# Kernel tuning notes

Measured on AMD Instinct MI355X. Metric: run time of the kernel, lower is better.

Reference implementation:

```python
import jax, jax.numpy as jnp
import numpy as np

B, N, D = 8, 2048, 256
K = 16384  # codebook_size


def setup_inputs() -> dict:
    key = jax.random.key(0)
    k1, k2, k3, k4 = jax.random.split(key, 4)
    z = jax.random.normal(k1, (B, N, D), dtype=jnp.float32)
    emb_weight = jax.random.normal(k2, (K, D), dtype=jnp.float32) * 0.02
    proj_w = jax.random.normal(k3, (D, D), dtype=jnp.float32) * (1.0 / np.sqrt(D))
    proj_b = jax.random.normal(k4, (D,), dtype=jnp.float32) * 0.01
    return {"z": z, "emb_weight": emb_weight, "proj_w": proj_w, "proj_b": proj_b}


def reference(z, emb_weight, proj_w, proj_b):
    # emb = embedding_proj(embedding.weight)  (torch Linear: x @ W^T + b)
    emb = emb_weight @ proj_w.T + proj_b  # (K, D)
    b, n, d = z.shape
    zf = z.reshape(b * n, d)  # (BN, D)
    # squared euclidean distances: ||z||^2 + ||e||^2 - 2 z e^T
    dist = (
        jnp.sum(zf * zf, axis=1, keepdims=True)
        + jnp.sum(emb * emb, axis=1)
        - 2.0 * jnp.einsum("bd,kd->bk", zf, emb)
    )  # (BN, K)
    q_indices = jnp.argmin(dist, axis=1)  # (BN,) int
    quantized = emb[q_indices].reshape(z.shape)  # (B, N, D)
    # straight-through estimator
    quantized = z + jax.lax.stop_gradient(quantized - z)
    q_indices = q_indices.reshape(b, n)
    # (unregularized_z, emb, regularized_z, bottleneck_rep)
    return z, emb, quantized, q_indices
```

## Files before the change

kernel.cpp:

```cpp
#include <hip/hip_runtime.h>
#include <hip/hip_bf16.h>

#define D      256
#define KCB    16384
#define BNROWS 16384
#define NT     4
#define MARGIN 0.15f
#define BIAS   8.0f
#define ZMAX   5.0f
#define EMAX   0.2f

typedef __attribute__((ext_vector_type(4))) int   int4v;
typedef __attribute__((ext_vector_type(4))) float f32x4;
typedef unsigned long long u64;

__device__ __forceinline__ void gload_lds16(const void* g, void* l) {
    __builtin_amdgcn_global_load_lds(
        (const __attribute__((address_space(1))) void*)g,
        (__attribute__((address_space(3))) void*)l, 16, 0, 0);
}

__device__ __forceinline__ unsigned fmap(float f) {
    unsigned u = __float_as_uint(f);
    return (u & 0x80000000u) ? ~u : (u | 0x80000000u);
}

__device__ __forceinline__ signed char q8(float x, float s) {
    return (signed char)__float2int_rn(fminf(fmaxf(x * s, -127.f), 127.f));
}

__global__ __launch_bounds__(256) void zquant_kernel(
    const float* __restrict__ z, signed char* __restrict__ z8)
{
    const int i = blockIdx.x * 256 + threadIdx.x;
    float4 v = ((const float4*)z)[i];
    const float s = 127.0f / ZMAX;
    char4 c;
    c.x = q8(v.x, s); c.y = q8(v.y, s); c.z = q8(v.z, s); c.w = q8(v.w, s);
    ((char4*)z8)[i] = c;
}

__global__ __launch_bounds__(256) void proj_kernel(
    const float* __restrict__ ew, const float* __restrict__ pw,
    const float* __restrict__ pb, float* __restrict__ emb)
{
    __shared__ float Et[64][65];
    __shared__ float Pt[64][65];
    const int tid = threadIdx.x;
    const int tc  = tid & 15, tr = tid >> 4;
    const int k0  = (blockIdx.x >> 2) * 64;
    const int d0  = (blockIdx.x & 3) * 64;

    float acc[4][4];
#pragma unroll
    for (int a = 0; a < 4; ++a)
#pragma unroll
        for (int b = 0; b < 4; ++b) acc[a][b] = 0.f;

    for (int j0 = 0; j0 < 256; j0 += 64) {
        __syncthreads();
#pragma unroll
        for (int i = 0; i < 4; ++i) {
            const int c = i * 256 + tid;
            const int r = c >> 4, c4 = (c & 15) * 4;
            float4 v = *(const float4*)(ew + (size_t)(k0 + r) * 256 + j0 + c4);
            Et[r][c4 + 0] = v.x; Et[r][c4 + 1] = v.y;
            Et[r][c4 + 2] = v.z; Et[r][c4 + 3] = v.w;
            float4 w = *(const float4*)(pw + (size_t)(d0 + r) * 256 + j0 + c4);
            Pt[r][c4 + 0] = w.x; Pt[r][c4 + 1] = w.y;
            Pt[r][c4 + 2] = w.z; Pt[r][c4 + 3] = w.w;
        }
        __syncthreads();
        for (int j = 0; j < 64; ++j) {
            float ev[4], pv[4];
#pragma unroll
            for (int a = 0; a < 4; ++a) ev[a] = Et[tr * 4 + a][j];
#pragma unroll
            for (int b = 0; b < 4; ++b) pv[b] = Pt[tc * 4 + b][j];
#pragma unroll
            for (int a = 0; a < 4; ++a)
#pragma unroll
                for (int b = 0; b < 4; ++b)
                    acc[a][b] = fmaf(ev[a], pv[b], acc[a][b]);
        }
    }

    const float4 bias = *(const float4*)(pb + d0 + tc * 4);
#pragma unroll
    for (int a = 0; a < 4; ++a) {
        float4 o;
        o.x = acc[a][0] + bias.x; o.y = acc[a][1] + bias.y;
        o.z = acc[a][2] + bias.z; o.w = acc[a][3] + bias.w;
        *(float4*)(emb + (size_t)(k0 + tr * 4 + a) * 256 + d0 + tc * 4) = o;
    }
}

__global__ __launch_bounds__(256) void snorm_equant_kernel(
    const float* __restrict__ emb, float* __restrict__ s,
    float* __restrict__ s8b, signed char* __restrict__ e8)
{
    const int tid = threadIdx.x;
    const int row = blockIdx.x * 64 + (tid >> 2);
    const int qd  = tid & 3;
    const size_t base = (size_t)row * 256;
    const float se = 127.0f / EMAX;
    float sq = 0.f;
#pragma unroll
    for (int j = 0; j < 16; ++j) {
        const int off = qd * 4 + j * 16;
        float4 v = *(const float4*)(emb + base + off);
        char4 c;
        c.x = q8(v.x, se); c.y = q8(v.y, se);
        c.z = q8(v.z, se); c.w = q8(v.w, se);
        *(char4*)(e8 + base + off) = c;
        sq = fmaf(v.x, v.x, fmaf(v.y, v.y, fmaf(v.z, v.z, fmaf(v.w, v.w, sq))));
    }
    sq += __shfl_xor(sq, 1);
    sq += __shfl_xor(sq, 2);
    if (qd == 0) {
        s[row]   = sq;
        s8b[row] = sq + BIAS;
    }
}

__global__ __launch_bounds__(512, 4) void argmin_hi_kernel(
    const signed char* __restrict__ z8, const signed char* __restrict__ e8,
    const float* __restrict__ s8b,
    unsigned* __restrict__ partial1, unsigned* __restrict__ partial2)
{
    __shared__ alignas(16) short A_lds[3 * 4096];
    __shared__ alignas(16) short B_lds[3 * 8192];

    const int tid  = threadIdx.x;
    const int lane = tid & 63;
    const int wid  = tid >> 6;
    const int wz   = wid >> 2;
    const int wc   = wid & 3;
    const int lcol = lane & 15;
    const int rhi  = lane >> 4;

    const int bm = blockIdx.x >> 6;
    const int bn = blockIdx.x & 63;
    const size_t r0 = (size_t)bm * 128;
    const size_t n0 = (size_t)bn * 256;

    const int slot  = (((lcol & 1) * 4 + rhi) ^ ((lcol >> 1) & 7)) << 3;
    const int aoff0 = wz * 2048 + (lcol >> 1) * 64 + slot;
    const int boff0 = wc * 2048 + (lcol >> 1) * 64 + slot;

    auto goff = [](int c) {
        const int l = c >> 3, u = (c & 7) ^ (l & 7);
        return (size_t)(2 * l + (u >> 2)) * 256 + (size_t)(u & 3) * 16;
    };
    const size_t gA  = goff(tid);
    const int    cB0 = wid * 128 + lane;
    const int    cB1 = cB0 + 64;
    const size_t gB0 = goff(cB0);
    const size_t gB1 = goff(cB1);

    short* const aDst  = A_lds + tid * 8;
    short* const bDst0 = B_lds + cB0 * 8;
    short* const bDst1 = B_lds + cB1 * 8;

    const char* const z8B = (const char*)z8 + r0 * 256;
    const char* const e8B = (const char*)e8 + n0 * 256;

    gload_lds16(z8B + gA, aDst);
    gload_lds16(e8B + gB0, bDst0);
    gload_lds16(e8B + gB1, bDst1);
    gload_lds16(z8B + 64 + gA, aDst + 4096);
    gload_lds16(e8B + 64 + gB0, bDst0 + 8192);
    gload_lds16(e8B + 64 + gB1, bDst1 + 8192);
    asm volatile("s_waitcnt vmcnt(3)" ::: "memory");
    __builtin_amdgcn_s_barrier();

    int4v acc[4][4];
    const int4v izero = {0, 0, 0, 0};
#pragma unroll
    for (int m = 0; m < 4; ++m)
#pragma unroll
        for (int n = 0; n < 4; ++n) acc[m][n] = izero;

#define TILE_BODY(JL)                                                         \
    {                                                                         \
        const int t  = i3 + (JL);                                             \
        const int tp = t + 2;                                                 \
        int4v bq[4];                                                          \
        _Pragma("unroll")                                                     \
        for (int n = 0; n < 4; ++n)            \
            bq[n] = *(const int4v*)(A_lds + (JL) * 4096 + aoff0 + n * 512);   \
        if (tp < NT) {                                                        \
            const char* Ab = z8B + ((size_t)tp << 6);                         \
            const char* Bb = e8B + ((size_t)tp << 6);                         \
            gload_lds16(Ab + gA, aDst + (((JL) + 2) % 3) * 4096);             \
            gload_lds16(Bb + gB0, bDst0 + (((JL) + 2) % 3) * 8192);           \
            gload_lds16(Bb + gB1, bDst1 + (((JL) + 2) % 3) * 8192);           \
        }                                                                     \
        __builtin_amdgcn_s_setprio(1);                                        \
        _Pragma("unroll")                                                     \
        for (int m = 0; m < 4; ++m) {       \
            const int4v am = *(const int4v*)(B_lds + (JL) * 8192 + boff0 + m * 512); \
            _Pragma("unroll")                                                 \
            for (int n = 0; n < 4; ++n)                                       \
                acc[m][n] = __builtin_amdgcn_mfma_i32_16x16x64_i8(            \
                    am, bq[n], acc[m][n], 0, 0, 0);                           \
        }                                                                     \
        __builtin_amdgcn_s_setprio(0);                                        \
        if (tp < NT)                                                          \
            asm volatile("s_waitcnt vmcnt(3)" ::: "memory");                  \
        else if (t + 1 < NT)                                                  \
            asm volatile("s_waitcnt vmcnt(0)" ::: "memory");                  \
        __builtin_amdgcn_s_barrier();                                         \
    }

    {
        const int i3 = 0;
        TILE_BODY(0)
        TILE_BODY(1)
        TILE_BODY(2)
    }
    {
        const int i3 = 3;
        TILE_BODY(0)
    }
#undef TILE_BODY

    const float FS2 = -2.0f * (ZMAX / 127.0f) * (EMAX / 127.0f);
    float4 s8[4];
#pragma unroll
    for (int mc = 0; mc < 4; ++mc)
        s8[mc] = *(const float4*)(s8b + n0 + wc * 64 + mc * 16 + rhi * 4);

    u64* cand = (u64*)A_lds;
#pragma unroll
    for (int nz = 0; nz < 4; ++nz) {
        unsigned v[16];
#pragma unroll
        for (int mc = 0; mc < 4; ++mc) {
            const unsigned cb = (unsigned)(wc * 64 + mc * 16 + rhi * 4);
            v[mc * 4 + 0] = (__float_as_uint(fmaf(FS2, (float)acc[mc][nz][0], s8[mc].x)) & 0xFFFFFF00u) | (cb + 0);
            v[mc * 4 + 1] = (__float_as_uint(fmaf(FS2, (float)acc[mc][nz][1], s8[mc].y)) & 0xFFFFFF00u) | (cb + 1);
            v[mc * 4 + 2] = (__float_as_uint(fmaf(FS2, (float)acc[mc][nz][2], s8[mc].z)) & 0xFFFFFF00u) | (cb + 2);
            v[mc * 4 + 3] = (__float_as_uint(fmaf(FS2, (float)acc[mc][nz][3], s8[mc].w)) & 0xFFFFFF00u) | (cb + 3);
        }
        unsigned p1 = min(v[0], v[1]), p2 = max(v[0], v[1]);
#pragma unroll
        for (int i = 1; i < 8; ++i) {
            const unsigned l = min(v[2 * i], v[2 * i + 1]);
            const unsigned h = max(v[2 * i], v[2 * i + 1]);
            const unsigned t = max(p1, l);
            p1 = min(p1, l);
            p2 = min(t, min(p2, h));
        }
#pragma unroll
        for (int mask = 16; mask <= 32; mask <<= 1) {
            const unsigned q1 = __shfl_xor(p1, mask);
            const unsigned q2 = __shfl_xor(p2, mask);
            const unsigned t  = max(p1, q1);
            p1 = min(p1, q1);
            p2 = min(t, min(p2, q2));
        }
        if (rhi == 0) {
            const int row = wz * 64 + nz * 16 + lcol;
            cand[row * 4 + wc] = (u64)p1 | ((u64)p2 << 32);
        }
    }
    __syncthreads();
    if (tid < 128) {
        const u64* c4 = cand + (size_t)tid * 4;
        u64 a = c4[0];
        unsigned p1 = (unsigned)a, p2 = (unsigned)(a >> 32);
#pragma unroll
        for (int w = 1; w < 4; ++w) {
            a = c4[w];
            const unsigned q1 = (unsigned)a, q2 = (unsigned)(a >> 32);
            const unsigned t  = max(p1, q1);
            p1 = min(p1, q1);
            p2 = min(t, min(p2, q2));
        }
        partial1[(size_t)bn * BNROWS + r0 + tid] = p1;
        partial2[(size_t)bn * BNROWS + r0 + tid] = p2;
    }
}

__global__ __launch_bounds__(256) void collect_rescore_kernel(
    const unsigned* __restrict__ partial1, const unsigned* __restrict__ partial2,
    const float* __restrict__ z, const float* __restrict__ emb,
    const float* __restrict__ s,
    float* __restrict__ outz, float* __restrict__ outq,
    float* __restrict__ outidx)
{
    __shared__ unsigned gsb;
    __shared__ int      nsel;
    __shared__ int      selk[128];
    __shared__ u64      wbest[4];
    __shared__ int      kfin;

    const int tid  = threadIdx.x;
    const int row  = blockIdx.x;
    const int lane = tid & 63;
    const int wid  = tid >> 6;

    unsigned v = 0xFFFFFFFFu;
    int vbn = 0;
    if (tid < 64)       { v = partial1[(size_t)tid * BNROWS + row];        vbn = tid; }
    else if (tid < 128) { v = partial2[(size_t)(tid - 64) * BNROWS + row]; vbn = tid - 64; }

    if (tid < 64) {
        unsigned g = v;
#pragma unroll
        for (int mm = 1; mm < 64; mm <<= 1) g = min(g, (unsigned)__shfl_xor(g, mm));
        if (tid == 0) { gsb = g; nsel = 0; }
    }
    __syncthreads();

    const float    gf  = __uint_as_float(gsb & 0xFFFFFF00u);
    const unsigned thr = __float_as_uint(gf + MARGIN) | 0xFFu;
    if (tid < 128 && v <= thr) {
        const int i = atomicAdd(&nsel, 1);
        selk[i] = vbn * 256 + (int)(v & 0xFFu);
    }
    __syncthreads();

    const float4 zv = *(const float4*)(z + (size_t)row * 256 + lane * 4);
    const int ns = nsel;
    u64 best = ~0ull;
    for (int i = wid; i < ns; i += 4) {
        const int k = selk[i];
        const float4 ev = *(const float4*)(emb + (size_t)k * 256 + lane * 4);
        float p = zv.x * ev.x;
        p = fmaf(zv.y, ev.y, p);
        p = fmaf(zv.z, ev.z, p);
        p = fmaf(zv.w, ev.w, p);
#pragma unroll
        for (int mm = 1; mm < 64; mm <<= 1) p += __shfl_xor(p, mm);
        const float sc = fmaf(-2.f, p, s[k]);
        const u64 pk = ((u64)fmap(sc) << 32) | (unsigned)k;
        best = (pk < best) ? pk : best;
    }
    if (lane == 0) wbest[wid] = best;
    __syncthreads();
    if (tid == 0) {
        u64 b = wbest[0];
        if (wbest[1] < b) b = wbest[1];
        if (wbest[2] < b) b = wbest[2];
        if (wbest[3] < b) b = wbest[3];
        kfin = (int)(b & 0xffffffffu);
        outidx[row] = (float)kfin;
    }
    __syncthreads();

    const int k = kfin;
    outz[(size_t)row * 256 + tid] = z[(size_t)row * 256 + tid];
    outq[(size_t)row * 256 + tid] = emb[(size_t)k * 256 + tid];
}

extern "C" void kernel_launch(void* const* d_in, const int* in_sizes, int n_in,
                              void* d_out, int out_size, void* d_ws, size_t ws_size,
                              hipStream_t stream)
{
    const float* z  = (const float*)d_in[0];
    const float* ew = (const float*)d_in[1];
    const float* pw = (const float*)d_in[2];
    const float* pb = (const float*)d_in[3];

    float* out     = (float*)d_out;
    float* out_z   = out;
    float* out_emb = out + (size_t)BNROWS * D;
    float* out_q   = out + 2 * (size_t)BNROWS * D;
    float* out_idx = out + 3 * (size_t)BNROWS * D;

    float*       sbuf  = (float*)d_ws;
    float*       s8b   = (float*)((char*)d_ws + 65536);
    signed char* z8    = (signed char*)((char*)d_ws + 131072);
    unsigned*    part1 = (unsigned*)((char*)d_ws + 131072 + 4194304);
    unsigned*    part2 = (unsigned*)((char*)d_ws + 131072 + 2 * 4194304);
    signed char* e8    = (signed char*)out_q;

    zquant_kernel<<<(BNROWS * D) / (256 * 4), 256, 0, stream>>>(z, z8);
    proj_kernel<<<(KCB / 64) * 4, 256, 0, stream>>>(ew, pw, pb, out_emb);
    snorm_equant_kernel<<<KCB / 64, 256, 0, stream>>>(out_emb, sbuf, s8b, e8);
    argmin_hi_kernel<<<(BNROWS / 128) * (KCB / 256), 512, 0, stream>>>(
        z8, e8, s8b, part1, part2);
    collect_rescore_kernel<<<BNROWS, 256, 0, stream>>>(
        part1, part2, z, out_emb, sbuf, out_z, out_q, out_idx);
}
```

Baseline: 180.5 us.

## Merge prep kernels and switch argmin candidate keys to integer arithmetic

The z quantization kernel and the codebook projection kernel become one launch, with the projection blocks also quantizing their outputs to int8. The separate norm kernel now only computes squared norms plus an integer-scaled bias. In the argmin epilogue, the per-element float FMA, bit cast and mask are replaced by an integer subtract of the int32 MFMA accumulator from the prescaled norm, shifted and packed with the column index. The margin threshold is likewise applied in integer units. This removes one launch and some epilogue ALU work, but the 24-bit integer key can wrap or lose precision if the accumulator range exceeds what the bias was chosen for.

```diff
diff --git a/kernel.cpp b/kernel.cpp
--- a/kernel.cpp
+++ b/kernel.cpp
@@ -1,14 +1,16 @@
 #include <hip/hip_runtime.h>
 #include <hip/hip_bf16.h>
 
-#define D      256
-#define KCB    16384
-#define BNROWS 16384
-#define NT     4
-#define MARGIN 0.15f
-#define BIAS   8.0f
-#define ZMAX   5.0f
-#define EMAX   0.2f
+#define D       256
+#define KCB     16384
+#define BNROWS  16384
+#define NT      4
+#define MARGIN  0.15f
+#define ZMAX    5.0f
+#define EMAX    0.2f
+#define FS2U    (2.0f * (ZMAX / 127.0f) * (EMAX / 127.0f))
+#define MARGIN_INT 1210u
+#define IBIAS   8388608
 
 typedef __attribute__((ext_vector_type(4))) int   int4v;
 typedef __attribute__((ext_vector_type(4))) float f32x4;
@@ -29,27 +31,30 @@
     return (signed char)__float2int_rn(fminf(fmaxf(x * s, -127.f), 127.f));
 }
 
-__global__ __launch_bounds__(256) void zquant_kernel(
-    const float* __restrict__ z, signed char* __restrict__ z8)
-{
-    const int i = blockIdx.x * 256 + threadIdx.x;
-    float4 v = ((const float4*)z)[i];
-    const float s = 127.0f / ZMAX;
-    char4 c;
-    c.x = q8(v.x, s); c.y = q8(v.y, s); c.z = q8(v.z, s); c.w = q8(v.w, s);
-    ((char4*)z8)[i] = c;
-}
-
-__global__ __launch_bounds__(256) void proj_kernel(
+__global__ __launch_bounds__(256) void prep_kernel(
+    const float* __restrict__ z, signed char* __restrict__ z8,
     const float* __restrict__ ew, const float* __restrict__ pw,
-    const float* __restrict__ pb, float* __restrict__ emb)
+    const float* __restrict__ pb, float* __restrict__ emb,
+    signed char* __restrict__ e8)
 {
     __shared__ float Et[64][65];
     __shared__ float Pt[64][65];
     const int tid = threadIdx.x;
+
+    if (blockIdx.x < 4096) {
+        const int i = blockIdx.x * 256 + tid;
+        float4 v = ((const float4*)z)[i];
+        const float s = 127.0f / ZMAX;
+        char4 c;
+        c.x = q8(v.x, s); c.y = q8(v.y, s); c.z = q8(v.z, s); c.w = q8(v.w, s);
+        ((char4*)z8)[i] = c;
+        return;
+    }
+
+    const int bid = blockIdx.x - 4096;
     const int tc  = tid & 15, tr = tid >> 4;
-    const int k0  = (blockIdx.x >> 2) * 64;
-    const int d0  = (blockIdx.x & 3) * 64;
+    const int k0  = (bid >> 2) * 64;
+    const int d0  = (bid & 3) * 64;
 
     float acc[4][4];
 #pragma unroll
@@ -86,46 +91,47 @@
     }
 
     const float4 bias = *(const float4*)(pb + d0 + tc * 4);
+    const float se = 127.0f / EMAX;
 #pragma unroll
     for (int a = 0; a < 4; ++a) {
         float4 o;
         o.x = acc[a][0] + bias.x; o.y = acc[a][1] + bias.y;
         o.z = acc[a][2] + bias.z; o.w = acc[a][3] + bias.w;
-        *(float4*)(emb + (size_t)(k0 + tr * 4 + a) * 256 + d0 + tc * 4) = o;
-    }
-}
-
-__global__ __launch_bounds__(256) void snorm_equant_kernel(
+        const size_t off = (size_t)(k0 + tr * 4 + a) * 256 + d0 + tc * 4;
+        *(float4*)(emb + off) = o;
+        char4 c;
+        c.x = q8(o.x, se); c.y = q8(o.y, se);
+        c.z = q8(o.z, se); c.w = q8(o.w, se);
+        *(char4*)(e8 + off) = c;
+    }
+}
+
+__global__ __launch_bounds__(256) void snorm_kernel(
     const float* __restrict__ emb, float* __restrict__ s,
-    float* __restrict__ s8b, signed char* __restrict__ e8)
+    int* __restrict__ s_bi)
 {
     const int tid = threadIdx.x;
     const int row = blockIdx.x * 64 + (tid >> 2);
     const int qd  = tid & 3;
     const size_t base = (size_t)row * 256;
-    const float se = 127.0f / EMAX;
     float sq = 0.f;
 #pragma unroll
     for (int j = 0; j < 16; ++j) {
         const int off = qd * 4 + j * 16;
         float4 v = *(const float4*)(emb + base + off);
-        char4 c;
-        c.x = q8(v.x, se); c.y = q8(v.y, se);
-        c.z = q8(v.z, se); c.w = q8(v.w, se);
-        *(char4*)(e8 + base + off) = c;
         sq = fmaf(v.x, v.x, fmaf(v.y, v.y, fmaf(v.z, v.z, fmaf(v.w, v.w, sq))));
     }
     sq += __shfl_xor(sq, 1);
     sq += __shfl_xor(sq, 2);
     if (qd == 0) {
-        s[row]   = sq;
-        s8b[row] = sq + BIAS;
+        s[row]    = sq;
+        s_bi[row] = (int)rintf(sq / FS2U) + IBIAS;
     }
 }
 
 __global__ __launch_bounds__(512, 4) void argmin_hi_kernel(
     const signed char* __restrict__ z8, const signed char* __restrict__ e8,
-    const float* __restrict__ s8b,
+    const int* __restrict__ s_bi,
     unsigned* __restrict__ partial1, unsigned* __restrict__ partial2)
 {
     __shared__ alignas(16) short A_lds[3 * 4096];
@@ -225,11 +231,10 @@
     }
 #undef TILE_BODY
 
-    const float FS2 = -2.0f * (ZMAX / 127.0f) * (EMAX / 127.0f);
-    float4 s8[4];
+    int4v sb[4];
 #pragma unroll
     for (int mc = 0; mc < 4; ++mc)
-        s8[mc] = *(const float4*)(s8b + n0 + wc * 64 + mc * 16 + rhi * 4);
+        sb[mc] = *(const int4v*)(s_bi + n0 + wc * 64 + mc * 16 + rhi * 4);
 
     u64* cand = (u64*)A_lds;
 #pragma unroll
@@ -238,10 +243,10 @@
 #pragma unroll
         for (int mc = 0; mc < 4; ++mc) {
             const unsigned cb = (unsigned)(wc * 64 + mc * 16 + rhi * 4);
-            v[mc * 4 + 0] = (__float_as_uint(fmaf(FS2, (float)acc[mc][nz][0], s8[mc].x)) & 0xFFFFFF00u) | (cb + 0);
-            v[mc * 4 + 1] = (__float_as_uint(fmaf(FS2, (float)acc[mc][nz][1], s8[mc].y)) & 0xFFFFFF00u) | (cb + 1);
-            v[mc * 4 + 2] = (__float_as_uint(fmaf(FS2, (float)acc[mc][nz][2], s8[mc].z)) & 0xFFFFFF00u) | (cb + 2);
-            v[mc * 4 + 3] = (__float_as_uint(fmaf(FS2, (float)acc[mc][nz][3], s8[mc].w)) & 0xFFFFFF00u) | (cb + 3);
+#pragma unroll
+            for (int j = 0; j < 4; ++j)
+                v[mc * 4 + j] =
+                    ((unsigned)(sb[mc][j] - acc[mc][nz][j]) << 8) | (cb + j);
         }
         unsigned p1 = min(v[0], v[1]), p2 = max(v[0], v[1]);
 #pragma unroll
@@ -314,8 +319,7 @@
     }
     __syncthreads();
 
-    const float    gf  = __uint_as_float(gsb & 0xFFFFFF00u);
-    const unsigned thr = __float_as_uint(gf + MARGIN) | 0xFFu;
+    const unsigned thr = (((gsb >> 8) + MARGIN_INT) << 8) | 0xFFu;
     if (tid < 128 && v <= thr) {
         const int i = atomicAdd(&nsel, 1);
         selk[i] = vbn * 256 + (int)(v & 0xFFu);
@@ -371,17 +375,16 @@
     float* out_idx = out + 3 * (size_t)BNROWS * D;
 
     float*       sbuf  = (float*)d_ws;
-    float*       s8b   = (float*)((char*)d_ws + 65536);
+    int*         s_bi  = (int*)((char*)d_ws + 65536);
     signed char* z8    = (signed char*)((char*)d_ws + 131072);
     unsigned*    part1 = (unsigned*)((char*)d_ws + 131072 + 4194304);
     unsigned*    part2 = (unsigned*)((char*)d_ws + 131072 + 2 * 4194304);
     signed char* e8    = (signed char*)out_q;
 
-    zquant_kernel<<<(BNROWS * D) / (256 * 4), 256, 0, stream>>>(z, z8);
-    proj_kernel<<<(KCB / 64) * 4, 256, 0, stream>>>(ew, pw, pb, out_emb);
-    snorm_equant_kernel<<<KCB / 64, 256, 0, stream>>>(out_emb, sbuf, s8b, e8);
+    prep_kernel<<<4096 + 1024, 256, 0, stream>>>(z, z8, ew, pw, pb, out_emb, e8);
+    snorm_kernel<<<KCB / 64, 256, 0, stream>>>(out_emb, sbuf, s_bi);
     argmin_hi_kernel<<<(BNROWS / 128) * (KCB / 256), 512, 0, stream>>>(
-        z8, e8, s8b, part1, part2);
+        z8, e8, s_bi, part1, part2);
     collect_rescore_kernel<<<BNROWS, 256, 0, stream>>>(
         part1, part2, z, out_emb, sbuf, out_z, out_q, out_idx);
 }
```

After: 180.0 us. No clear change (-0.3%).
